# Optimization experiments

Measured on AMD Instinct MI355X. Metric: run time of the kernel, lower is better.

Reference implementation:

```python
import jax, jax.numpy as jnp
import numpy as np

B, S, D, H, DK = 4, 1024, 1024, 16, 64  # batch, seq (nq=nk=max_seq_len), d_model, heads, d_kqv
NEG = -1e9
BERN_P = 0.3


def setup_inputs() -> dict:
    key = jax.random.key(0)
    ks = jax.random.split(key, 12)
    xavier = lambda k, fi, fo: jax.random.uniform(k, (fi, fo), minval=-1.0, maxval=1.0) * np.sqrt(6.0 / (fi + fo))
    return {
        "x": jax.random.normal(ks[0], (B, S, D), dtype=jnp.float32),
        "mask": jax.random.randint(ks[1], (B, S), 0, 2).astype(bool),
        "pos_att": jax.random.normal(ks[2], (B, S, S), dtype=jnp.float32),
        "decoder_mask": 1,
        "Wq": xavier(ks[3], D, H * DK), "bq": jnp.zeros((H * DK,), jnp.float32),
        "Wk": xavier(ks[4], D, H * DK), "bk": jnp.zeros((H * DK,), jnp.float32),
        "Wv": xavier(ks[5], D, H * DK), "bv": jnp.zeros((H * DK,), jnp.float32),
        "Wo": xavier(ks[6], H * DK, D), "bo": jnp.zeros((D,), jnp.float32),
    }


def _forward(x, pos_att, Wq, bq, Wk, bk, Wv, bv, Wo, bo, mask, decoder_mask):
    b_s, nq, _ = x.shape
    nk = nq  # self-attention
    relu = jax.nn.relu
    # projections (Linear + activation), split into heads
    q = relu(x @ Wq + bq).reshape(b_s, nq, H, DK).transpose(0, 2, 1, 3)  # [b,h,q,d]
    k = relu(x @ Wk + bk).reshape(b_s, nk, H, DK).transpose(0, 2, 1, 3)  # [b,h,k,d]
    v = relu(x @ Wv + bv).reshape(b_s, nk, H, DK).transpose(0, 2, 1, 3)  # [b,h,k,d]
    att = jnp.einsum("bhqd,bhkd->bhqk", q, k) / np.sqrt(DK).astype(np.float32)
    # positional bias broadcast over heads
    att = att + pos_att[:, None, :, :]
    # bernoulli(0.3) noise: each kept score gets -1e9 added (deterministic key)
    bern = jax.random.bernoulli(jax.random.key(42), BERN_P, att.shape)
    att = att + bern.astype(att.dtype) * NEG
    # key-padding mask [b,1,1,nk]
    att = jnp.where(mask[:, None, None, :], NEG, att)
    # causal triu mask (decoder_mask=True path)
    if decoder_mask:
        tri = jnp.triu(jnp.ones((nq, nk), dtype=bool), k=1)
        att = jnp.where(tri[None, None, :, :], NEG, att)
    att = jax.nn.softmax(att, axis=-1)
    out = jnp.einsum("bhqk,bhkd->bqhd", att, v).reshape(b_s, nq, H * DK)
    out = relu(out @ Wo + bo)
    return out


def reference(x, mask, pos_att, decoder_mask, Wq, bq, Wk, bk, Wv, bv, Wo, bo):
    return _forward(x, pos_att, Wq, bq, Wk, bk, Wv, bv, Wo, bo, mask, decoder_mask)
```

## Files before the change

kernel.cpp:

```cpp
#include <hip/hip_runtime.h>
#include <hip/hip_bf16.h>

#define NEGV (-1e9f)

typedef __attribute__((ext_vector_type(4))) float f32x4;
typedef __attribute__((ext_vector_type(8))) short short8;

#define MFMA_BF16(a, b, c) __builtin_amdgcn_mfma_f32_16x16x32_bf16((a), (b), (c), 0, 0, 0)

#define GLOAD_LDS16(gsrc, ldst)                                                        \
    __builtin_amdgcn_global_load_lds(                                                  \
        (const __attribute__((address_space(1))) unsigned int*)(gsrc),                 \
        (__attribute__((address_space(3))) unsigned int*)(ldst), 16, 0, 0)

#define GLOAD_LDS4(gsrc, ldst)                                                         \
    __builtin_amdgcn_global_load_lds(                                                  \
        (const __attribute__((address_space(1))) unsigned int*)(gsrc),                 \
        (__attribute__((address_space(3))) unsigned int*)(ldst), 4, 0, 0)

__device__ __forceinline__ unsigned short f2bf(float f) {
    union { float f; unsigned u; } v; v.f = f;
    return (unsigned short)((v.u + 0x7fffu + ((v.u >> 16) & 1u)) >> 16);
}

__device__ __forceinline__ float bf2f(unsigned short u) {
    return __uint_as_float((unsigned)u << 16);
}

__device__ __forceinline__ unsigned rotl32(unsigned x, int r) {
    return (x << r) | (x >> (32 - r));
}

__device__ __forceinline__ bool bern_hit(unsigned idx) {
    const unsigned ks0 = 0u, ks1 = 42u, ks2 = 0x1BD11BDAu ^ 0u ^ 42u;
    unsigned x0 = ks0, x1 = idx + ks1;
#define TFR(r) { x0 += x1; x1 = rotl32(x1, (r)); x1 ^= x0; }
    TFR(13) TFR(15) TFR(26) TFR(6)   x0 += ks1; x1 += ks2 + 1u;
    TFR(17) TFR(29) TFR(16) TFR(24)  x0 += ks2; x1 += ks0 + 2u;
    TFR(13) TFR(15) TFR(26) TFR(6)   x0 += ks0; x1 += ks1 + 3u;
    TFR(17) TFR(29) TFR(16) TFR(24)  x0 += ks1; x1 += ks2 + 4u;
    TFR(13) TFR(15) TFR(26) TFR(6)   x0 += ks2; x1 += ks0 + 5u;
#undef TFR
    unsigned bits = x0 ^ x1;
    float u = __uint_as_float((bits >> 9) | 0x3f800000u) - 1.0f;
    return u < 0.3f;
}

__global__ void prep_mask_kernel(const unsigned* __restrict__ mraw,
                                 int* __restrict__ mcanon) {
    __shared__ int f_gt1, f_nonfloatish, f_oddnz;
    const int t = threadIdx.x;
    if (t == 0) { f_gt1 = 0; f_nonfloatish = 0; f_oddnz = 0; }
    __syncthreads();
    unsigned w = mraw[t];
    if (w > 1u) f_gt1 = 1;
    if (w != 0u && w != 1u && w != 0x3f800000u) f_nonfloatish = 1;
    if ((t & 1) && w != 0u) f_oddnz = 1;
    __syncthreads();
    int mode;
    if (!f_gt1)              mode = f_oddnz ? 0 : 3;
    else if (!f_nonfloatish) mode = 2;
    else                     mode = 1;
    for (int i = t; i < 4096; i += 1024) {
        int v;
        if (mode == 0)      v = (int)mraw[i];
        else if (mode == 1) v = ((const unsigned char*)mraw)[i] ? 1 : 0;
        else if (mode == 2) v = (mraw[i] != 0u) ? 1 : 0;
        else                v = (mraw[2 * i] != 0u) ? 1 : 0;
        mcanon[i] = v;
    }
}

__global__ __launch_bounds__(256) void conv_x_kernel(const float* __restrict__ in,
                                                     unsigned short* __restrict__ out) {
    const int i = (blockIdx.x * 256 + threadIdx.x) * 4;
    float4 v = *reinterpret_cast<const float4*>(&in[i]);
    ushort4 o;
    o.x = f2bf(v.x); o.y = f2bf(v.y); o.z = f2bf(v.z); o.w = f2bf(v.w);
    *reinterpret_cast<ushort4*>(&out[i]) = o;
}

__global__ __launch_bounds__(256) void conv_wt_kernel(const float* __restrict__ W,
                                                      unsigned short* __restrict__ WT) {
    __shared__ float ts[64][68];
    const int t = threadIdx.x;
    const int k0 = blockIdx.y * 64, n0 = blockIdx.x * 64;
    const int r = t >> 4, c4 = (t & 15) * 4;
#pragma unroll
    for (int rr = 0; rr < 4; ++rr) {
        const int row = r + rr * 16;
        float4 v = *reinterpret_cast<const float4*>(&W[(size_t)(k0 + row) * 1024 + n0 + c4]);
        ts[row][c4 + 0] = v.x; ts[row][c4 + 1] = v.y;
        ts[row][c4 + 2] = v.z; ts[row][c4 + 3] = v.w;
    }
    __syncthreads();
#pragma unroll
    for (int rr = 0; rr < 4; ++rr) {
        const int n = r + rr * 16;
        ushort4 o;
        o.x = f2bf(ts[c4 + 0][n]); o.y = f2bf(ts[c4 + 1][n]);
        o.z = f2bf(ts[c4 + 2][n]); o.w = f2bf(ts[c4 + 3][n]);
        *reinterpret_cast<ushort4*>(&WT[(size_t)(n0 + n) * 1024 + k0 + c4]) = o;
    }
}

template<int WRITE_BF16>
__global__ __launch_bounds__(256) void gemm_bf16(
    const unsigned short* __restrict__ A, const unsigned short* __restrict__ BT,
    const float* __restrict__ bias, void* __restrict__ Cout,
    int M, int N, int K) {
    __shared__ unsigned short As[8192];
    __shared__ unsigned short Bs[8192];
    const int t = threadIdx.x;
    const int lane = t & 63, w = t >> 6;
    const int wr = w >> 1, wc = w & 1;
    const int lgrp = lane >> 4, l15 = lane & 15;
    const int m0 = blockIdx.y * 128, n0 = blockIdx.x * 128;
    const int srow = t >> 3;
    const int scol = ((t & 7) ^ (srow & 7)) << 3;
    const int rdsw = (l15 & 7) << 4;
    f32x4 acc[4][4] = {};

    for (int k0 = 0; k0 < K; k0 += 64) {
#pragma unroll
        for (int s = 0; s < 4; ++s) {
            GLOAD_LDS16(&A[(size_t)(m0 + s * 32 + srow) * K + (k0 + scol)], &As[s * 2048 + t * 8]);
            GLOAD_LDS16(&BT[(size_t)(n0 + s * 32 + srow) * K + (k0 + scol)], &Bs[s * 2048 + t * 8]);
        }
        __syncthreads();
#pragma unroll
        for (int kkh = 0; kkh < 2; ++kkh) {
            const int klb = (kkh * 32 + (lgrp << 3)) * 2;
            short8 af[4], bf[4];
#pragma unroll
            for (int i = 0; i < 4; ++i) {
                af[i] = *(const short8*)((const char*)As + (wr * 64 + i * 16 + l15) * 128 + (klb ^ rdsw));
                bf[i] = *(const short8*)((const char*)Bs + (wc * 64 + i * 16 + l15) * 128 + (klb ^ rdsw));
            }
#pragma unroll
            for (int mf = 0; mf < 4; ++mf)
#pragma unroll
                for (int nf = 0; nf < 4; ++nf)
                    acc[mf][nf] = MFMA_BF16(af[mf], bf[nf], acc[mf][nf]);
        }
        __syncthreads();
    }
#pragma unroll
    for (int nf = 0; nf < 4; ++nf) {
        const int n = n0 + wc * 64 + nf * 16 + l15;
        const float bv = bias[n];
#pragma unroll
        for (int mf = 0; mf < 4; ++mf) {
#pragma unroll
            for (int r = 0; r < 4; ++r) {
                const int m = m0 + wr * 64 + mf * 16 + (lgrp << 2) + r;
                float v = fmaxf(acc[mf][nf][r] + bv, 0.f);
                if (WRITE_BF16) ((unsigned short*)Cout)[(size_t)m * N + n] = f2bf(v);
                else            ((float*)Cout)[(size_t)m * N + n] = v;
            }
        }
    }
}

__global__ __launch_bounds__(256) void vsum_part(const unsigned short* __restrict__ Vb,
                                                 float* __restrict__ part) {
    const int c = blockIdx.x, b = blockIdx.y, t = threadIdx.x;
    float a0 = 0, a1 = 0, a2 = 0, a3 = 0;
    const unsigned short* src = &Vb[((size_t)(b * 1024 + c * 64)) * 1024 + t * 4];
    for (int r = 0; r < 64; ++r) {
        ushort4 v = *(const ushort4*)(src + (size_t)r * 1024);
        a0 += bf2f(v.x); a1 += bf2f(v.y); a2 += bf2f(v.z); a3 += bf2f(v.w);
    }
    float4 o = {a0, a1, a2, a3};
    *(float4*)&part[(size_t)(b * 16 + c) * 1024 + t * 4] = o;
}

__global__ __launch_bounds__(256) void vsum_reduce(const float* __restrict__ part,
                                                   float* __restrict__ vmean) {
    const int b = blockIdx.x, t = threadIdx.x;
    float4 s = {0, 0, 0, 0};
    for (int c = 0; c < 16; ++c) {
        float4 v = *(const float4*)&part[(size_t)(b * 16 + c) * 1024 + t * 4];
        s.x += v.x; s.y += v.y; s.z += v.z; s.w += v.w;
    }
    const float sc = 1.0f / 1024.0f;
    float4 o = {s.x * sc, s.y * sc, s.z * sc, s.w * sc};
    *(float4*)&vmean[b * 1024 + t * 4] = o;
}

__global__ __launch_bounds__(256) void attn_kernel(
    const unsigned short* __restrict__ Qb, const unsigned short* __restrict__ Kb,
    const unsigned short* __restrict__ Vb, const float* __restrict__ pos,
    const int* __restrict__ mcanon, const unsigned* __restrict__ dec,
    const float* __restrict__ vmean, unsigned short* __restrict__ AO) {
    const int g = blockIdx.x, h = blockIdx.y, b = blockIdx.z;
    const int t = threadIdx.x, lane = t & 63, w = t >> 6;
    const int lgrp = lane >> 4, l15 = lane & 15;

    __shared__ unsigned short Ks[4096];
    __shared__ unsigned short VT[4096];
    __shared__ float pos_s[4096];
    __shared__ int mask_s[64];

    const int dm = (dec[0] != 0u) ? 1 : 0;

    for (int ph = 0; ph < 2; ++ph) {
        const int qt = ph ? (15 - g) : g;
        const int q0 = qt * 64;
        const int ntiles = dm ? (qt + 1) : 16;
        const int qi = q0 + w * 16 + l15;

        const size_t qg = ((size_t)(b * 1024 + qi)) * 1024 + h * 64 + (lgrp << 3);
        const short8 qb0 = *(const short8*)&Qb[qg];
        const short8 qb1 = *(const short8*)&Qb[qg + 32];

        float m = -3e38f, l = 0.f;
        f32x4 osc[4] = {};

        for (int kt = 0; kt < ntiles; ++kt) {
            const int kbase = kt * 64;
            {
                const int srow = t >> 3;
                const int scol = ((t & 7) ^ (srow & 7)) << 3;
                GLOAD_LDS16(&Kb[((size_t)(b * 1024 + kbase + srow)) * 1024 + h * 64 + scol],
                            &Ks[t * 8]);
                GLOAD_LDS16(&Kb[((size_t)(b * 1024 + kbase + 32 + srow)) * 1024 + h * 64 + scol],
                            &Ks[2048 + t * 8]);
            }
#pragma unroll
            for (int s = 0; s < 4; ++s) {
                const int row = w * 16 + s * 4 + (lane >> 4);
                const int scol = ((lane & 15) ^ (row & 15)) << 2;
                GLOAD_LDS16(&pos[((size_t)(b * 1024 + q0 + row)) * 1024 + kbase + scol],
                            &pos_s[w * 1024 + s * 256 + lane * 4]);
            }
            if (w == 0) GLOAD_LDS4(&mcanon[b * 1024 + kbase + lane], &mask_s[lane]);
            {
                const int p = t >> 3;
                const int dblk = (t & 7) << 3;
                const unsigned short* vs = &Vb[((size_t)(b * 1024 + kbase + 2 * p)) * 1024 + h * 64 + dblk];
                short8 v0 = *(const short8*)vs;
                short8 v1 = *(const short8*)(vs + 1024);
#pragma unroll
                for (int j = 0; j < 8; ++j) {
                    const int d = dblk + j;
                    const int sw = (d & 7) ^ ((d >> 3) & 7);
                    unsigned word = (unsigned)(unsigned short)v0[j] |
                                    ((unsigned)(unsigned short)v1[j] << 16);
                    *(unsigned*)((char*)VT + d * 128 + ((((2 * p) >> 3) ^ sw) << 4) +
                                 (((2 * p) & 7) << 1)) = word;
                }
            }
            __syncthreads();

            f32x4 sacc[4] = {};
#pragma unroll
            for (int kkh = 0; kkh < 2; ++kkh) {
                const int klb = (kkh * 32 + (lgrp << 3)) * 2;
                const short8 qf = kkh ? qb1 : qb0;
#pragma unroll
                for (int f = 0; f < 4; ++f) {
                    short8 kf = *(const short8*)((const char*)Ks + (f * 16 + l15) * 128 +
                                                 (klb ^ ((l15 & 7) << 4)));
                    sacc[f] = MFMA_BF16(kf, qf, sacc[f]);
                }
            }

            float p16[4][4];
            float tmax = -3e38f;
#pragma unroll
            for (int f = 0; f < 4; ++f) {
                const f32x4 posq = *(const f32x4*)&pos_s[(w * 16 + l15) * 64 +
                                                         (((f * 4 + lgrp) ^ l15) << 2)];
                const int4 mq = *(const int4*)&mask_s[f * 16 + (lgrp << 2)];
                const int mqa[4] = {mq.x, mq.y, mq.z, mq.w};
#pragma unroll
                for (int r = 0; r < 4; ++r) {
                    const int ki = kbase + f * 16 + (lgrp << 2) + r;
                    float lg = NEGV;
                    const bool live = (mqa[r] == 0) && !(dm && (ki > qi));
                    if (live) {
                        float sc = fmaf(sacc[f][r], 0.125f, posq[r]);
                        if (bern_hit((((unsigned)((b * 16 + h) * 1024 + qi)) << 10) + (unsigned)ki))
                            sc += NEGV;
                        lg = sc;
                    }
                    p16[f][r] = lg;
                    tmax = fmaxf(tmax, lg);
                }
            }
            tmax = fmaxf(tmax, __shfl_xor(tmax, 16, 64));
            tmax = fmaxf(tmax, __shfl_xor(tmax, 32, 64));
            const float mn = fmaxf(m, tmax);
            const float fac = expf(m - mn);

            float psum = 0.f;
            unsigned pk[4][2];
#pragma unroll
            for (int f = 0; f < 4; ++f) {
#pragma unroll
                for (int rr = 0; rr < 2; ++rr) {
                    float pa = expf(p16[f][2 * rr] - mn);
                    float pb = expf(p16[f][2 * rr + 1] - mn);
                    psum += pa + pb;
                    pk[f][rr] = (unsigned)f2bf(pa) | ((unsigned)f2bf(pb) << 16);
                }
            }
            psum += __shfl_xor(psum, 16, 64);
            psum += __shfl_xor(psum, 32, 64);
            l = l * fac + psum;
            m = mn;

#pragma unroll
            for (int r = 0; r < 4; ++r) {
                const float fr = __int_as_float(__builtin_amdgcn_ds_bpermute(
                    (((lgrp << 2) + r) << 2), __float_as_int(fac)));
#pragma unroll
                for (int nf = 0; nf < 4; ++nf) osc[nf][r] *= fr;
            }

            {
                const int idx0 = ((((lgrp << 1) & 3) << 4) | l15) << 2;
                const int idx1 = (((((lgrp << 1) + 1) & 3) << 4) | l15) << 2;
                const bool hi = (lgrp >> 1) != 0;
#pragma unroll
                for (int kkh = 0; kkh < 2; ++kkh) {
                    union { unsigned u[4]; short8 s; } pa;
#pragma unroll
                    for (int s2 = 0; s2 < 4; ++s2) {
                        const int rr = s2 & 1;
                        const int idx = (s2 >> 1) ? idx1 : idx0;
                        const unsigned lo = (unsigned)__builtin_amdgcn_ds_bpermute(idx, (int)pk[kkh * 2][rr]);
                        const unsigned hw = (unsigned)__builtin_amdgcn_ds_bpermute(idx, (int)pk[kkh * 2 + 1][rr]);
                        pa.u[s2] = hi ? hw : lo;
                    }
#pragma unroll
                    for (int nf = 0; nf < 4; ++nf) {
                        const int d = nf * 16 + l15;
                        const int sw = (d & 7) ^ ((d >> 3) & 7);
                        short8 vf = *(const short8*)((const char*)VT + d * 128 +
                                                     ((((kkh << 2) + lgrp) ^ sw) << 4));
                        osc[nf] = MFMA_BF16(pa.s, vf, osc[nf]);
                    }
                }
            }
            __syncthreads();
        }

#pragma unroll
        for (int r = 0; r < 4; ++r) {
            const int src = (((lgrp << 2) + r) << 2);
            const float lr = __int_as_float(__builtin_amdgcn_ds_bpermute(src, __float_as_int(l)));
            const float mr = __int_as_float(__builtin_amdgcn_ds_bpermute(src, __float_as_int(m)));
            const int qo = q0 + w * 16 + (lgrp << 2) + r;
            const bool dgen = (mr == NEGV);
            const float inv = 1.0f / lr;
#pragma unroll
            for (int nf = 0; nf < 4; ++nf) {
                const int d = nf * 16 + l15;
                float v = dgen ? vmean[b * 1024 + h * 64 + d] : osc[nf][r] * inv;
                AO[((size_t)(b * 1024 + qo)) * 1024 + h * 64 + d] = f2bf(v);
            }
        }
        __syncthreads();
    }
}

extern "C" void kernel_launch(void* const* d_in, const int* in_sizes, int n_in,
                              void* d_out, int out_size, void* d_ws, size_t ws_size,
                              hipStream_t stream) {
    const float* x       = (const float*)d_in[0];
    const unsigned* mraw = (const unsigned*)d_in[1];
    const float* pos     = (const float*)d_in[2];
    const unsigned* dec  = (const unsigned*)d_in[3];
    const float* Wq = (const float*)d_in[4];  const float* bq = (const float*)d_in[5];
    const float* Wk = (const float*)d_in[6];  const float* bk = (const float*)d_in[7];
    const float* Wv = (const float*)d_in[8];  const float* bv = (const float*)d_in[9];
    const float* Wo = (const float*)d_in[10]; const float* bo = (const float*)d_in[11];
    float* out = (float*)d_out;

    char* ws = (char*)d_ws;
    unsigned short* xb  = (unsigned short*)(ws);
    unsigned short* wtq = (unsigned short*)(ws + (8u  << 20));
    unsigned short* wtk = (unsigned short*)(ws + (10u << 20));
    unsigned short* wtv = (unsigned short*)(ws + (12u << 20));
    unsigned short* wto = (unsigned short*)(ws + (14u << 20));
    unsigned short* Qb  = (unsigned short*)(ws + (16u << 20));
    unsigned short* Kb  = (unsigned short*)(ws + (24u << 20));
    unsigned short* Vb  = (unsigned short*)(ws + (32u << 20));
    unsigned short* AO  = (unsigned short*)(ws + (40u << 20));
    int* mcanon         = (int*)(ws + (48u << 20));
    float* part  = (float*)(ws);
    float* vmean = (float*)(ws + (1u << 19));

    prep_mask_kernel<<<1, 1024, 0, stream>>>(mraw, mcanon);
    conv_x_kernel<<<4096, 256, 0, stream>>>(x, xb);
    dim3 tg(16, 16);
    conv_wt_kernel<<<tg, 256, 0, stream>>>(Wq, wtq);
    conv_wt_kernel<<<tg, 256, 0, stream>>>(Wk, wtk);
    conv_wt_kernel<<<tg, 256, 0, stream>>>(Wv, wtv);
    conv_wt_kernel<<<tg, 256, 0, stream>>>(Wo, wto);

    dim3 gg(8, 32);
    gemm_bf16<1><<<gg, 256, 0, stream>>>(xb, wtq, bq, Qb, 4096, 1024, 1024);
    gemm_bf16<1><<<gg, 256, 0, stream>>>(xb, wtk, bk, Kb, 4096, 1024, 1024);
    gemm_bf16<1><<<gg, 256, 0, stream>>>(xb, wtv, bv, Vb, 4096, 1024, 1024);

    vsum_part<<<dim3(16, 4), 256, 0, stream>>>(Vb, part);
    vsum_reduce<<<4, 256, 0, stream>>>(part, vmean);

    attn_kernel<<<dim3(8, 16, 4), 256, 0, stream>>>(Qb, Kb, Vb, pos, mcanon, dec, vmean, AO);

    gemm_bf16<0><<<gg, 256, 0, stream>>>(AO, wto, bo, out, 4096, 1024, 1024);
}
```

Measured before the change: 331.9 us.

## Precompute bernoulli bitmask, fuse QKV GEMM, rebalance attention grid and output GEMM tiles

Several changes at once. The Threefry bernoulli draws move out of the attention inner loop into a separate kernel that stores one 64-bit ballot mask per row and key tile, and attention reads that mask. Q, K and V projections become one concatenated GEMM with a concatenated bias and a split write. The attention grid now gives each block a single query tile, assigned through a permutation table, instead of a paired front/back schedule, and uses fast __expf. The output GEMM switches to 64-row tiles to launch more blocks. These changes add extra launches and a mask buffer, and single-tile blocks may balance load differently under the causal mask.

```diff
diff --git a/kernel.cpp b/kernel.cpp
--- a/kernel.cpp
+++ b/kernel.cpp
@@ -27,14 +27,10 @@
     return __uint_as_float((unsigned)u << 16);
 }
 
-__device__ __forceinline__ unsigned rotl32(unsigned x, int r) {
-    return (x << r) | (x >> (32 - r));
-}
-
 __device__ __forceinline__ bool bern_hit(unsigned idx) {
     const unsigned ks0 = 0u, ks1 = 42u, ks2 = 0x1BD11BDAu ^ 0u ^ 42u;
     unsigned x0 = ks0, x1 = idx + ks1;
-#define TFR(r) { x0 += x1; x1 = rotl32(x1, (r)); x1 ^= x0; }
+#define TFR(r) { x0 += x1; x1 = __builtin_rotateleft32(x1, (unsigned)(r)); x1 ^= x0; }
     TFR(13) TFR(15) TFR(26) TFR(6)   x0 += ks1; x1 += ks2 + 1u;
     TFR(17) TFR(29) TFR(16) TFR(24)  x0 += ks2; x1 += ks0 + 2u;
     TFR(13) TFR(15) TFR(26) TFR(6)   x0 += ks0; x1 += ks1 + 3u;
@@ -44,6 +40,29 @@
     unsigned bits = x0 ^ x1;
     float u = __uint_as_float((bits >> 9) | 0x3f800000u) - 1.0f;
     return u < 0.3f;
+}
+
+__global__ __launch_bounds__(256) void bern_kernel(const unsigned* __restrict__ dec,
+                                                   unsigned long long* __restrict__ bw) {
+    const int W = (blockIdx.x * 256 + threadIdx.x) >> 6;
+    const int lane = threadIdx.x & 63;
+    const int dm = (dec[0] != 0u) ? 1 : 0;
+    for (int j = 0; j < 8; ++j) {
+        const int p = W * 8 + j;
+        const int bh = p >> 9;
+        const int q = p & 511;
+#pragma unroll
+        for (int s = 0; s < 2; ++s) {
+            const int qq = s ? (1023 - q) : q;
+            const int row = (bh << 10) + qq;
+            const int nw = dm ? ((qq >> 6) + 1) : 16;
+            for (int kw = 0; kw < nw; ++kw) {
+                const unsigned idx = ((unsigned)row << 10) + (unsigned)(kw << 6) + (unsigned)lane;
+                const unsigned long long word = __ballot(bern_hit(idx));
+                if (lane == 0) bw[(size_t)row * 16 + kw] = word;
+            }
+        }
+    }
 }
 
 __global__ void prep_mask_kernel(const unsigned* __restrict__ mraw,
@@ -104,41 +123,49 @@
     }
 }
 
-template<int WRITE_BF16>
+__global__ void concat_bias_kernel(const float* __restrict__ a, const float* __restrict__ b,
+                                   const float* __restrict__ c, float* __restrict__ o) {
+    const int i = blockIdx.x * 256 + threadIdx.x;
+    o[i] = (i < 1024) ? a[i] : ((i < 2048) ? b[i - 1024] : c[i - 2048]);
+}
+
+template<int MF, int WMODE>
 __global__ __launch_bounds__(256) void gemm_bf16(
     const unsigned short* __restrict__ A, const unsigned short* __restrict__ BT,
     const float* __restrict__ bias, void* __restrict__ Cout,
     int M, int N, int K) {
-    __shared__ unsigned short As[8192];
+    __shared__ unsigned short As[MF * 2048];
     __shared__ unsigned short Bs[8192];
     const int t = threadIdx.x;
     const int lane = t & 63, w = t >> 6;
     const int wr = w >> 1, wc = w & 1;
     const int lgrp = lane >> 4, l15 = lane & 15;
-    const int m0 = blockIdx.y * 128, n0 = blockIdx.x * 128;
+    const int m0 = blockIdx.y * (MF * 32), n0 = blockIdx.x * 128;
     const int srow = t >> 3;
     const int scol = ((t & 7) ^ (srow & 7)) << 3;
     const int rdsw = (l15 & 7) << 4;
-    f32x4 acc[4][4] = {};
+    f32x4 acc[MF][4] = {};
 
     for (int k0 = 0; k0 < K; k0 += 64) {
 #pragma unroll
-        for (int s = 0; s < 4; ++s) {
+        for (int s = 0; s < MF; ++s)
             GLOAD_LDS16(&A[(size_t)(m0 + s * 32 + srow) * K + (k0 + scol)], &As[s * 2048 + t * 8]);
+#pragma unroll
+        for (int s = 0; s < 4; ++s)
             GLOAD_LDS16(&BT[(size_t)(n0 + s * 32 + srow) * K + (k0 + scol)], &Bs[s * 2048 + t * 8]);
-        }
         __syncthreads();
 #pragma unroll
         for (int kkh = 0; kkh < 2; ++kkh) {
             const int klb = (kkh * 32 + (lgrp << 3)) * 2;
-            short8 af[4], bf[4];
-#pragma unroll
-            for (int i = 0; i < 4; ++i) {
-                af[i] = *(const short8*)((const char*)As + (wr * 64 + i * 16 + l15) * 128 + (klb ^ rdsw));
+            short8 af[MF], bf[4];
+#pragma unroll
+            for (int i = 0; i < MF; ++i)
+                af[i] = *(const short8*)((const char*)As + (wr * (MF * 16) + i * 16 + l15) * 128 + (klb ^ rdsw));
+#pragma unroll
+            for (int i = 0; i < 4; ++i)
                 bf[i] = *(const short8*)((const char*)Bs + (wc * 64 + i * 16 + l15) * 128 + (klb ^ rdsw));
-            }
-#pragma unroll
-            for (int mf = 0; mf < 4; ++mf)
+#pragma unroll
+            for (int mf = 0; mf < MF; ++mf)
 #pragma unroll
                 for (int nf = 0; nf < 4; ++nf)
                     acc[mf][nf] = MFMA_BF16(af[mf], bf[nf], acc[mf][nf]);
@@ -150,13 +177,19 @@
         const int n = n0 + wc * 64 + nf * 16 + l15;
         const float bv = bias[n];
 #pragma unroll
-        for (int mf = 0; mf < 4; ++mf) {
+        for (int mf = 0; mf < MF; ++mf) {
 #pragma unroll
             for (int r = 0; r < 4; ++r) {
-                const int m = m0 + wr * 64 + mf * 16 + (lgrp << 2) + r;
+                const int m = m0 + wr * (MF * 16) + mf * 16 + (lgrp << 2) + r;
                 float v = fmaxf(acc[mf][nf][r] + bv, 0.f);
-                if (WRITE_BF16) ((unsigned short*)Cout)[(size_t)m * N + n] = f2bf(v);
-                else            ((float*)Cout)[(size_t)m * N + n] = v;
+                if (WMODE == 0) {
+                    ((float*)Cout)[(size_t)m * N + n] = v;
+                } else if (WMODE == 1) {
+                    ((unsigned short*)Cout)[(size_t)m * N + n] = f2bf(v);
+                } else {
+                    const int which = n >> 10;
+                    ((unsigned short*)Cout)[(size_t)which * 4194304u + (size_t)m * 1024 + (n & 1023)] = f2bf(v);
+                }
             }
         }
     }
@@ -192,8 +225,9 @@
     const unsigned short* __restrict__ Qb, const unsigned short* __restrict__ Kb,
     const unsigned short* __restrict__ Vb, const float* __restrict__ pos,
     const int* __restrict__ mcanon, const unsigned* __restrict__ dec,
-    const float* __restrict__ vmean, unsigned short* __restrict__ AO) {
-    const int g = blockIdx.x, h = blockIdx.y, b = blockIdx.z;
+    const unsigned long long* __restrict__ bern, const float* __restrict__ vmean,
+    unsigned short* __restrict__ AO) {
+    const int gx = blockIdx.x, h = blockIdx.y, b = blockIdx.z;
     const int t = threadIdx.x, lane = t & 63, w = t >> 6;
     const int lgrp = lane >> 4, l15 = lane & 15;
 
@@ -203,166 +237,165 @@
     __shared__ int mask_s[64];
 
     const int dm = (dec[0] != 0u) ? 1 : 0;
-
-    for (int ph = 0; ph < 2; ++ph) {
-        const int qt = ph ? (15 - g) : g;
-        const int q0 = qt * 64;
-        const int ntiles = dm ? (qt + 1) : 16;
-        const int qi = q0 + w * 16 + l15;
-
-        const size_t qg = ((size_t)(b * 1024 + qi)) * 1024 + h * 64 + (lgrp << 3);
-        const short8 qb0 = *(const short8*)&Qb[qg];
-        const short8 qb1 = *(const short8*)&Qb[qg + 32];
-
-        float m = -3e38f, l = 0.f;
-        f32x4 osc[4] = {};
-
-        for (int kt = 0; kt < ntiles; ++kt) {
-            const int kbase = kt * 64;
-            {
-                const int srow = t >> 3;
-                const int scol = ((t & 7) ^ (srow & 7)) << 3;
-                GLOAD_LDS16(&Kb[((size_t)(b * 1024 + kbase + srow)) * 1024 + h * 64 + scol],
-                            &Ks[t * 8]);
-                GLOAD_LDS16(&Kb[((size_t)(b * 1024 + kbase + 32 + srow)) * 1024 + h * 64 + scol],
-                            &Ks[2048 + t * 8]);
-            }
-#pragma unroll
-            for (int s = 0; s < 4; ++s) {
-                const int row = w * 16 + s * 4 + (lane >> 4);
-                const int scol = ((lane & 15) ^ (row & 15)) << 2;
-                GLOAD_LDS16(&pos[((size_t)(b * 1024 + q0 + row)) * 1024 + kbase + scol],
-                            &pos_s[w * 1024 + s * 256 + lane * 4]);
-            }
-            if (w == 0) GLOAD_LDS4(&mcanon[b * 1024 + kbase + lane], &mask_s[lane]);
-            {
-                const int p = t >> 3;
-                const int dblk = (t & 7) << 3;
-                const unsigned short* vs = &Vb[((size_t)(b * 1024 + kbase + 2 * p)) * 1024 + h * 64 + dblk];
-                short8 v0 = *(const short8*)vs;
-                short8 v1 = *(const short8*)(vs + 1024);
-#pragma unroll
-                for (int j = 0; j < 8; ++j) {
-                    const int d = dblk + j;
+    const int qt = (int)((0x765489AB3210CDEFull >> (((gx + 4 * b) & 15) << 2)) & 15);
+    const int q0 = qt * 64;
+    const int ntiles = dm ? (qt + 1) : 16;
+    const int qi = q0 + w * 16 + l15;
+
+    const size_t qg = ((size_t)(b * 1024 + qi)) * 1024 + h * 64 + (lgrp << 3);
+    const short8 qb0 = *(const short8*)&Qb[qg];
+    const short8 qb1 = *(const short8*)&Qb[qg + 32];
+    const unsigned browbase = ((unsigned)((b * 16 + h) * 1024 + qi)) * 16u;
+
+    float m = -3e38f, l = 0.f;
+    f32x4 osc[4] = {};
+    const int qor = w * 16 + (lgrp << 2);
+
+    for (int kt = 0; kt < ntiles; ++kt) {
+        const int kbase = kt * 64;
+        {
+            const int srow = t >> 3;
+            const int scol = ((t & 7) ^ (srow & 7)) << 3;
+            GLOAD_LDS16(&Kb[((size_t)(b * 1024 + kbase + srow)) * 1024 + h * 64 + scol],
+                        &Ks[t * 8]);
+            GLOAD_LDS16(&Kb[((size_t)(b * 1024 + kbase + 32 + srow)) * 1024 + h * 64 + scol],
+                        &Ks[2048 + t * 8]);
+        }
+#pragma unroll
+        for (int s = 0; s < 4; ++s) {
+            const int row = w * 16 + s * 4 + (lane >> 4);
+            const int scol = ((lane & 15) ^ (row & 15)) << 2;
+            GLOAD_LDS16(&pos[((size_t)(b * 1024 + q0 + row)) * 1024 + kbase + scol],
+                        &pos_s[w * 1024 + s * 256 + lane * 4]);
+        }
+        if (w == 0) GLOAD_LDS4(&mcanon[b * 1024 + kbase + lane], &mask_s[lane]);
+        const unsigned long long bwv = bern[browbase + kt];
+        {
+            const int p = t >> 3;
+            const int dblk = (t & 7) << 3;
+            const unsigned short* vs = &Vb[((size_t)(b * 1024 + kbase + 2 * p)) * 1024 + h * 64 + dblk];
+            short8 v0 = *(const short8*)vs;
+            short8 v1 = *(const short8*)(vs + 1024);
+#pragma unroll
+            for (int j = 0; j < 8; ++j) {
+                const int d = dblk + j;
+                const int sw = (d & 7) ^ ((d >> 3) & 7);
+                unsigned word = (unsigned)(unsigned short)v0[j] |
+                                ((unsigned)(unsigned short)v1[j] << 16);
+                *(unsigned*)((char*)VT + d * 128 + ((((2 * p) >> 3) ^ sw) << 4) +
+                             (((2 * p) & 7) << 1)) = word;
+            }
+        }
+        __syncthreads();
+
+        f32x4 sacc[4] = {};
+#pragma unroll
+        for (int kkh = 0; kkh < 2; ++kkh) {
+            const int klb = (kkh * 32 + (lgrp << 3)) * 2;
+            const short8 qf = kkh ? qb1 : qb0;
+#pragma unroll
+            for (int f = 0; f < 4; ++f) {
+                short8 kf = *(const short8*)((const char*)Ks + (f * 16 + l15) * 128 +
+                                             (klb ^ ((l15 & 7) << 4)));
+                sacc[f] = MFMA_BF16(kf, qf, sacc[f]);
+            }
+        }
+
+        float p16[4][4];
+        float tmax = -3e38f;
+#pragma unroll
+        for (int f = 0; f < 4; ++f) {
+            const f32x4 posq = *(const f32x4*)&pos_s[(w * 16 + l15) * 64 +
+                                                     (((f * 4 + lgrp) ^ l15) << 2)];
+            const int4 mq = *(const int4*)&mask_s[f * 16 + (lgrp << 2)];
+            const int mqa[4] = {mq.x, mq.y, mq.z, mq.w};
+            const unsigned nib = (unsigned)(bwv >> (f * 16 + (lgrp << 2))) & 0xFu;
+#pragma unroll
+            for (int r = 0; r < 4; ++r) {
+                const int ki = kbase + f * 16 + (lgrp << 2) + r;
+                float lg = NEGV;
+                const bool live = (mqa[r] == 0) && !(dm && (ki > qi));
+                if (live) {
+                    float sc = fmaf(sacc[f][r], 0.125f, posq[r]);
+                    sc += ((nib >> r) & 1u) ? NEGV : 0.f;
+                    lg = sc;
+                }
+                p16[f][r] = lg;
+                tmax = fmaxf(tmax, lg);
+            }
+        }
+        tmax = fmaxf(tmax, __shfl_xor(tmax, 16, 64));
+        tmax = fmaxf(tmax, __shfl_xor(tmax, 32, 64));
+        const float mn = fmaxf(m, tmax);
+        const float fac = __expf(m - mn);
+
+        float psum = 0.f;
+        unsigned pk[4][2];
+#pragma unroll
+        for (int f = 0; f < 4; ++f) {
+#pragma unroll
+            for (int rr = 0; rr < 2; ++rr) {
+                float pa = __expf(p16[f][2 * rr] - mn);
+                float pb = __expf(p16[f][2 * rr + 1] - mn);
+                psum += pa + pb;
+                pk[f][rr] = (unsigned)f2bf(pa) | ((unsigned)f2bf(pb) << 16);
+            }
+        }
+        psum += __shfl_xor(psum, 16, 64);
+        psum += __shfl_xor(psum, 32, 64);
+        l = l * fac + psum;
+        m = mn;
+
+#pragma unroll
+        for (int r = 0; r < 4; ++r) {
+            const float fr = __int_as_float(__builtin_amdgcn_ds_bpermute(
+                (((lgrp << 2) + r) << 2), __float_as_int(fac)));
+#pragma unroll
+            for (int nf = 0; nf < 4; ++nf) osc[nf][r] *= fr;
+        }
+
+        {
+            const int idx0 = ((((lgrp << 1) & 3) << 4) | l15) << 2;
+            const int idx1 = (((((lgrp << 1) + 1) & 3) << 4) | l15) << 2;
+            const bool hi = (lgrp >> 1) != 0;
+#pragma unroll
+            for (int kkh = 0; kkh < 2; ++kkh) {
+                union { unsigned u[4]; short8 s; } pa;
+#pragma unroll
+                for (int s2 = 0; s2 < 4; ++s2) {
+                    const int rr = s2 & 1;
+                    const int idx = (s2 >> 1) ? idx1 : idx0;
+                    const unsigned lo = (unsigned)__builtin_amdgcn_ds_bpermute(idx, (int)pk[kkh * 2][rr]);
+                    const unsigned hw = (unsigned)__builtin_amdgcn_ds_bpermute(idx, (int)pk[kkh * 2 + 1][rr]);
+                    pa.u[s2] = hi ? hw : lo;
+                }
+#pragma unroll
+                for (int nf = 0; nf < 4; ++nf) {
+                    const int d = nf * 16 + l15;
                     const int sw = (d & 7) ^ ((d >> 3) & 7);
-                    unsigned word = (unsigned)(unsigned short)v0[j] |
-                                    ((unsigned)(unsigned short)v1[j] << 16);
-                    *(unsigned*)((char*)VT + d * 128 + ((((2 * p) >> 3) ^ sw) << 4) +
-                                 (((2 * p) & 7) << 1)) = word;
+                    short8 vf = *(const short8*)((const char*)VT + d * 128 +
+                                                 ((((kkh << 2) + lgrp) ^ sw) << 4));
+                    osc[nf] = MFMA_BF16(pa.s, vf, osc[nf]);
                 }
             }
-            __syncthreads();
-
-            f32x4 sacc[4] = {};
-#pragma unroll
-            for (int kkh = 0; kkh < 2; ++kkh) {
-                const int klb = (kkh * 32 + (lgrp << 3)) * 2;
-                const short8 qf = kkh ? qb1 : qb0;
-#pragma unroll
-                for (int f = 0; f < 4; ++f) {
-                    short8 kf = *(const short8*)((const char*)Ks + (f * 16 + l15) * 128 +
-                                                 (klb ^ ((l15 & 7) << 4)));
-                    sacc[f] = MFMA_BF16(kf, qf, sacc[f]);
-                }
-            }
-
-            float p16[4][4];
-            float tmax = -3e38f;
-#pragma unroll
-            for (int f = 0; f < 4; ++f) {
-                const f32x4 posq = *(const f32x4*)&pos_s[(w * 16 + l15) * 64 +
-                                                         (((f * 4 + lgrp) ^ l15) << 2)];
-                const int4 mq = *(const int4*)&mask_s[f * 16 + (lgrp << 2)];
-                const int mqa[4] = {mq.x, mq.y, mq.z, mq.w};
-#pragma unroll
-                for (int r = 0; r < 4; ++r) {
-                    const int ki = kbase + f * 16 + (lgrp << 2) + r;
-                    float lg = NEGV;
-                    const bool live = (mqa[r] == 0) && !(dm && (ki > qi));
-                    if (live) {
-                        float sc = fmaf(sacc[f][r], 0.125f, posq[r]);
-                        if (bern_hit((((unsigned)((b * 16 + h) * 1024 + qi)) << 10) + (unsigned)ki))
-                            sc += NEGV;
-                        lg = sc;
-                    }
-                    p16[f][r] = lg;
-                    tmax = fmaxf(tmax, lg);
-                }
-            }
-            tmax = fmaxf(tmax, __shfl_xor(tmax, 16, 64));
-            tmax = fmaxf(tmax, __shfl_xor(tmax, 32, 64));
-            const float mn = fmaxf(m, tmax);
-            const float fac = expf(m - mn);
-
-            float psum = 0.f;
-            unsigned pk[4][2];
-#pragma unroll
-            for (int f = 0; f < 4; ++f) {
-#pragma unroll
-                for (int rr = 0; rr < 2; ++rr) {
-                    float pa = expf(p16[f][2 * rr] - mn);
-                    float pb = expf(p16[f][2 * rr + 1] - mn);
-                    psum += pa + pb;
-                    pk[f][rr] = (unsigned)f2bf(pa) | ((unsigned)f2bf(pb) << 16);
-                }
-            }
-            psum += __shfl_xor(psum, 16, 64);
-            psum += __shfl_xor(psum, 32, 64);
-            l = l * fac + psum;
-            m = mn;
-
-#pragma unroll
-            for (int r = 0; r < 4; ++r) {
-                const float fr = __int_as_float(__builtin_amdgcn_ds_bpermute(
-                    (((lgrp << 2) + r) << 2), __float_as_int(fac)));
-#pragma unroll
-                for (int nf = 0; nf < 4; ++nf) osc[nf][r] *= fr;
-            }
-
-            {
-                const int idx0 = ((((lgrp << 1) & 3) << 4) | l15) << 2;
-                const int idx1 = (((((lgrp << 1) + 1) & 3) << 4) | l15) << 2;
-                const bool hi = (lgrp >> 1) != 0;
-#pragma unroll
-                for (int kkh = 0; kkh < 2; ++kkh) {
-                    union { unsigned u[4]; short8 s; } pa;
-#pragma unroll
-                    for (int s2 = 0; s2 < 4; ++s2) {
-                        const int rr = s2 & 1;
-                        const int idx = (s2 >> 1) ? idx1 : idx0;
-                        const unsigned lo = (unsigned)__builtin_amdgcn_ds_bpermute(idx, (int)pk[kkh * 2][rr]);
-                        const unsigned hw = (unsigned)__builtin_amdgcn_ds_bpermute(idx, (int)pk[kkh * 2 + 1][rr]);
-                        pa.u[s2] = hi ? hw : lo;
-                    }
-#pragma unroll
-                    for (int nf = 0; nf < 4; ++nf) {
-                        const int d = nf * 16 + l15;
-                        const int sw = (d & 7) ^ ((d >> 3) & 7);
-                        short8 vf = *(const short8*)((const char*)VT + d * 128 +
-                                                     ((((kkh << 2) + lgrp) ^ sw) << 4));
-                        osc[nf] = MFMA_BF16(pa.s, vf, osc[nf]);
-                    }
-                }
-            }
-            __syncthreads();
-        }
-
-#pragma unroll
-        for (int r = 0; r < 4; ++r) {
-            const int src = (((lgrp << 2) + r) << 2);
-            const float lr = __int_as_float(__builtin_amdgcn_ds_bpermute(src, __float_as_int(l)));
-            const float mr = __int_as_float(__builtin_amdgcn_ds_bpermute(src, __float_as_int(m)));
-            const int qo = q0 + w * 16 + (lgrp << 2) + r;
-            const bool dgen = (mr == NEGV);
-            const float inv = 1.0f / lr;
-#pragma unroll
-            for (int nf = 0; nf < 4; ++nf) {
-                const int d = nf * 16 + l15;
-                float v = dgen ? vmean[b * 1024 + h * 64 + d] : osc[nf][r] * inv;
-                AO[((size_t)(b * 1024 + qo)) * 1024 + h * 64 + d] = f2bf(v);
-            }
         }
         __syncthreads();
+    }
+
+#pragma unroll
+    for (int r = 0; r < 4; ++r) {
+        const int src = (((lgrp << 2) + r) << 2);
+        const float lr = __int_as_float(__builtin_amdgcn_ds_bpermute(src, __float_as_int(l)));
+        const float mr = __int_as_float(__builtin_amdgcn_ds_bpermute(src, __float_as_int(m)));
+        const int qo = q0 + qor + r;
+        const bool dgen = (mr == NEGV);
+        const float inv = 1.0f / lr;
+#pragma unroll
+        for (int nf = 0; nf < 4; ++nf) {
+            const int d = nf * 16 + l15;
+            float v = dgen ? vmean[b * 1024 + h * 64 + d] : osc[nf][r] * inv;
+            AO[((size_t)(b * 1024 + qo)) * 1024 + h * 64 + d] = f2bf(v);
+        }
     }
 }
 
@@ -380,36 +413,35 @@
     float* out = (float*)d_out;
 
     char* ws = (char*)d_ws;
-    unsigned short* xb  = (unsigned short*)(ws);
-    unsigned short* wtq = (unsigned short*)(ws + (8u  << 20));
-    unsigned short* wtk = (unsigned short*)(ws + (10u << 20));
-    unsigned short* wtv = (unsigned short*)(ws + (12u << 20));
-    unsigned short* wto = (unsigned short*)(ws + (14u << 20));
-    unsigned short* Qb  = (unsigned short*)(ws + (16u << 20));
-    unsigned short* Kb  = (unsigned short*)(ws + (24u << 20));
-    unsigned short* Vb  = (unsigned short*)(ws + (32u << 20));
-    unsigned short* AO  = (unsigned short*)(ws + (40u << 20));
-    int* mcanon         = (int*)(ws + (48u << 20));
+    unsigned short* xb   = (unsigned short*)(ws);
+    unsigned short* wcat = (unsigned short*)(ws + (8u << 20));
+    unsigned short* wto  = wcat + 3u * 1024 * 1024;
+    float* bcat          = (float*)(ws + (16u << 20));
+    int* mcanon          = (int*)(ws + (16u << 20) + (64u << 10));
+    unsigned short* Qb   = (unsigned short*)(ws + (17u << 20));
+    unsigned short* Kb   = Qb + 4u * 1024 * 1024;
+    unsigned short* Vb   = Qb + 8u * 1024 * 1024;
+    unsigned short* AO   = (unsigned short*)(ws + (41u << 20));
+    unsigned long long* bern = (unsigned long long*)(ws + (49u << 20));
     float* part  = (float*)(ws);
     float* vmean = (float*)(ws + (1u << 19));
 
     prep_mask_kernel<<<1, 1024, 0, stream>>>(mraw, mcanon);
+    bern_kernel<<<1024, 256, 0, stream>>>(dec, bern);
     conv_x_kernel<<<4096, 256, 0, stream>>>(x, xb);
     dim3 tg(16, 16);
-    conv_wt_kernel<<<tg, 256, 0, stream>>>(Wq, wtq);
-    conv_wt_kernel<<<tg, 256, 0, stream>>>(Wk, wtk);
-    conv_wt_kernel<<<tg, 256, 0, stream>>>(Wv, wtv);
+    conv_wt_kernel<<<tg, 256, 0, stream>>>(Wq, wcat);
+    conv_wt_kernel<<<tg, 256, 0, stream>>>(Wk, wcat + 1024u * 1024u);
+    conv_wt_kernel<<<tg, 256, 0, stream>>>(Wv, wcat + 2u * 1024u * 1024u);
     conv_wt_kernel<<<tg, 256, 0, stream>>>(Wo, wto);
-
-    dim3 gg(8, 32);
-    gemm_bf16<1><<<gg, 256, 0, stream>>>(xb, wtq, bq, Qb, 4096, 1024, 1024);
-    gemm_bf16<1><<<gg, 256, 0, stream>>>(xb, wtk, bk, Kb, 4096, 1024, 1024);
-    gemm_bf16<1><<<gg, 256, 0, stream>>>(xb, wtv, bv, Vb, 4096, 1024, 1024);
+    concat_bias_kernel<<<12, 256, 0, stream>>>(bq, bk, bv, bcat);
+
+    gemm_bf16<4, 2><<<dim3(24, 32), 256, 0, stream>>>(xb, wcat, bcat, Qb, 4096, 3072, 1024);
 
     vsum_part<<<dim3(16, 4), 256, 0, stream>>>(Vb, part);
     vsum_reduce<<<4, 256, 0, stream>>>(part, vmean);
 
-    attn_kernel<<<dim3(8, 16, 4), 256, 0, stream>>>(Qb, Kb, Vb, pos, mcanon, dec, vmean, AO);
-
-    gemm_bf16<0><<<gg, 256, 0, stream>>>(AO, wto, bo, out, 4096, 1024, 1024);
-}
+    attn_kernel<<<dim3(16, 16, 4), 256, 0, stream>>>(Qb, Kb, Vb, pos, mcanon, dec, bern, vmean, AO);
+
+    gemm_bf16<2, 0><<<dim3(8, 64), 256, 0, stream>>>(AO, wto, bo, out, 4096, 1024, 1024);
+}
```

Result: slower. 340.5 us (+2.6%).
